# Performance work log

Measured on AMD Instinct MI355X. Metric: run time of the kernel, lower is better.

The kernel has to match this reference:

```python
import jax, jax.numpy as jnp
import numpy as np

def setup_inputs() -> dict:
    key = jax.random.key(0)
    k1, k2, k3, k4 = jax.random.split(key, 4)
    B, S, E, H = 4, 4096, 1024, 64
    x = jax.random.normal(k1, (B, S, E), dtype=jnp.float32)
    scale = E ** -0.5  # keep activations well-scaled like trained Linear weights
    Wq = jax.random.normal(k2, (E, H), dtype=jnp.float32) * scale
    Wk = jax.random.normal(k3, (E, H), dtype=jnp.float32) * scale
    Wv = jax.random.normal(k4, (E, H), dtype=jnp.float32) * scale
    return {"x": x, "Wq": Wq, "Wk": Wk, "Wv": Wv}

def reference(x, Wq, Wk, Wv):
    # x: [B, S, E]; W*: [E, H]
    B, S, E = x.shape
    H = Wq.shape[1]
    q = jnp.einsum('bse,eh->bsh', x, Wq)
    k = jnp.einsum('bse,eh->bsh', x, Wk)
    v = jnp.einsum('bse,eh->bsh', x, Wv)
    att = jnp.einsum('bqh,bkh->bqk', q, k) * (H ** -0.5)  # [B, S, S]
    causal = jnp.tril(jnp.ones((S, S), dtype=bool))
    att = jnp.where(causal, att, -jnp.inf)
    att = jax.nn.softmax(att, axis=-1)
    # dropout p=0.0 (eval-mode): identity
    return jnp.einsum('bqk,bkh->bqh', att, v)
```

## Files before the change

kernel.cpp:

```cpp
#include <hip/hip_runtime.h>


using short8 = __attribute__((ext_vector_type(8))) short;
using f32x4  = __attribute__((ext_vector_type(4))) float;

#define MFMA16(A, B, C) __builtin_amdgcn_mfma_f32_16x16x32_bf16((A), (B), (C), 0, 0, 0)

typedef const __attribute__((address_space(1))) void* gas_ptr;
typedef __attribute__((address_space(3))) void*       las_ptr;

__device__ __forceinline__ void gload16(const void* g, void* l) {
    __builtin_amdgcn_global_load_lds((gas_ptr)g, (las_ptr)l, 16, 0, 0);
}

__device__ __forceinline__ unsigned short f2bf(float f) {
    unsigned u = __builtin_bit_cast(unsigned, f);
    u += 0x7fffu + ((u >> 16) & 1u);
    return (unsigned short)(u >> 16);
}
__device__ __forceinline__ float bf2f(unsigned short u) {
    unsigned v = ((unsigned)u) << 16;
    return __builtin_bit_cast(float, v);
}

__device__ __forceinline__ float exp2_fast(float x) {
#if __has_builtin(__builtin_amdgcn_exp2f)
    return __builtin_amdgcn_exp2f(x);
#else
    float r;
    asm("v_exp_f32 %0, %1" : "=v"(r) : "v"(x));
    return r;
#endif
}

__global__ __launch_bounds__(256) void transpose_w(
    const float* __restrict__ Wq,
    const float* __restrict__ Wk,
    const float* __restrict__ Wv,
    unsigned short* __restrict__ Ws)
{
    int o = blockIdx.x * 256 + threadIdx.x;
    if (o < 196608) {
        int j    = o & 7;
        int l    = (o >> 3) & 63;
        int g    = (o >> 9) & 7;
        int rem  = o >> 12;
        int mt   = rem % 3;
        int sk   = rem / 3;
        int c    = g >> 2, nt = g & 3;
        int quad = l >> 4, n  = l & 15;
        int e    = sk * 64 + c * 32 + quad * 8 + j;
        int h    = nt * 16 + n;
        const float* W = (mt == 0) ? Wq : (mt == 1) ? Wk : Wv;
        Ws[o] = f2bf(W[e * 64 + h]);
    }
}

__global__ __launch_bounds__(128, 2) void proj_all(
    const float* __restrict__ x,
    const unsigned short* __restrict__ Ws,
    unsigned short* __restrict__ Qo,
    unsigned short* __restrict__ Ko,
    unsigned short* __restrict__ Vto)
{
    const int m0   = blockIdx.x * 32;
    const int tid  = threadIdx.x;
    const int lane = tid & 63;
    const int wv   = tid >> 6;
    const int quad = lane >> 4;
    const int n    = lane & 15;

    __shared__ __align__(16) float xs[2][8][64][4];
    __shared__ __align__(16) short wf[2][24][64][8];

    const f32x4 zero4 = {0.f, 0.f, 0.f, 0.f};
    f32x4 acc[3][4];
    #pragma unroll
    for (int mt = 0; mt < 3; ++mt)
        #pragma unroll
        for (int nt = 0; nt < 4; ++nt) acc[mt][nt] = zero4;

    auto stage = [&](int k0, int p) {
        #pragma unroll
        for (int it = 0; it < 4; ++it) {
            int i     = wv + 2 * it;
            int Rl    = 4 * i + (lane >> 4);
            int chunk = (lane & 15) ^ ((Rl & 3) << 2);
            gload16(x + (size_t)(m0 + Rl) * 1024 + k0 + chunk * 4, &xs[p][i][0][0]);
        }
        int sk = k0 >> 6;
        #pragma unroll
        for (int it = 0; it < 12; ++it) {
            int f = wv + 2 * it;
            gload16(Ws + (((size_t)sk * 24 + f) << 9) + lane * 8, &wf[p][f][0][0]);
        }
    };

    int p = 0;
    stage(0, 0);
    __syncthreads();

    for (int k0 = 0; k0 < 1024; k0 += 64) {
        if (k0 < 960) stage(k0 + 64, p ^ 1);

        int sub = n & 3, s = sub << 2;
        const float* xp = &xs[p][wv * 4 + (n >> 2)][0][0] + sub * 64;
        f32x4 u0 = *(const f32x4*)(xp + (((2 * quad)     ^ s) << 2));
        f32x4 u1 = *(const f32x4*)(xp + (((2 * quad + 1) ^ s) << 2));
        f32x4 u2 = *(const f32x4*)(xp + (((8 + 2 * quad) ^ s) << 2));
        f32x4 u3 = *(const f32x4*)(xp + (((9 + 2 * quad) ^ s) << 2));
        short8 a0, a1;
        #pragma unroll
        for (int j = 0; j < 4; ++j) {
            a0[j]     = (short)f2bf(u0[j]);
            a0[4 + j] = (short)f2bf(u1[j]);
            a1[j]     = (short)f2bf(u2[j]);
            a1[4 + j] = (short)f2bf(u3[j]);
        }

        #pragma unroll
        for (int mt = 0; mt < 3; ++mt)
            #pragma unroll
            for (int nt = 0; nt < 4; ++nt) {
                acc[mt][nt] = MFMA16(a0, *(const short8*)(&wf[p][mt * 8 + nt][lane][0]),     acc[mt][nt]);
                acc[mt][nt] = MFMA16(a1, *(const short8*)(&wf[p][mt * 8 + 4 + nt][lane][0]), acc[mt][nt]);
            }

        __syncthreads();
        p ^= 1;
    }

    #pragma unroll
    for (int nt = 0; nt < 4; ++nt) {
        #pragma unroll
        for (int r = 0; r < 4; ++r) {
            int m = m0 + wv * 16 + quad * 4 + r;
            int h = nt * 16 + n;
            Qo[(size_t)m * 64 + h] = f2bf(acc[0][nt][r]);
            Ko[(size_t)m * 64 + h] = f2bf(acc[1][nt][r]);
            int b = m >> 12, s2 = m & 4095;
            Vto[((size_t)(b * 80 + h)) * 4096 + s2] = f2bf(acc[2][nt][r]);
        }
    }
}

template <int SPLIT>
__device__ __forceinline__ void attn_body(
    const unsigned short* __restrict__ Q,
    const unsigned short* __restrict__ K,
    const unsigned short* __restrict__ Vt,
    float* __restrict__ dst,
    int b, int r0, int kt0, int kt1)
{
    const int tid  = threadIdx.x;
    const int lane = tid & 63;
    const int wv   = tid >> 6;
    const int quad = lane >> 4;
    const int n    = lane & 15;
    const int ktmask = r0 >> 6;

    __shared__ __align__(16) short kf[2][8][64][8];
    __shared__ __align__(16) short vf[2][8][64][8];
    __shared__ __align__(16) unsigned short pbuf[4][32][72];

    short8 qa[2][2];
    #pragma unroll
    for (int rg = 0; rg < 2; ++rg) {
        const unsigned short* qp =
            Q + (size_t)(b * 4096 + r0 + wv * 32 + rg * 16 + n) * 64 + quad * 8;
        #pragma unroll
        for (int j = 0; j < 8; ++j) {
            qa[rg][0][j] = (short)f2bf(bf2f(qp[j])      * 0.18033688f);
            qa[rg][1][j] = (short)f2bf(bf2f(qp[32 + j]) * 0.18033688f);
        }
    }

    const f32x4 zero4 = {0.f, 0.f, 0.f, 0.f};
    f32x4 oacc[2][4];
    float lacc[2][4];
    #pragma unroll
    for (int rg = 0; rg < 2; ++rg)
        #pragma unroll
        for (int nt = 0; nt < 4; ++nt) { oacc[rg][nt] = zero4; lacc[rg][nt] = 0.f; }

    const unsigned short* kbase = K  + ((size_t)b * 4096 + n) * 64 + quad * 8;
    const unsigned short* vbase = Vt + ((size_t)b * 80 + n) * 4096 + quad * 8;

    auto stage = [&](int kt, int p) {
        #pragma unroll
        for (int it = 0; it < 4; ++it) {
            int f = wv + 4 * it;
            if (f < 8) {
                int c = f >> 2, nt = f & 3;
                gload16(kbase + (size_t)(kt * 64 + nt * 16) * 64 + c * 32, &kf[p][f][0][0]);
            } else {
                int pnl = f - 8;
                int nt = pnl >> 1, c = pnl & 1;
                gload16(vbase + (size_t)nt * 16 * 4096 + kt * 64 + c * 32, &vf[p][pnl][0][0]);
            }
        }
    };

    int p = 0;
    stage(kt0, 0);
    __syncthreads();

    for (int kt = kt0; kt <= kt1; ++kt) {
        if (kt < kt1) stage(kt + 1, p ^ 1);

        f32x4 sacc[2][4];
        #pragma unroll
        for (int rg = 0; rg < 2; ++rg)
            #pragma unroll
            for (int nt = 0; nt < 4; ++nt) sacc[rg][nt] = zero4;

        #pragma unroll
        for (int nt = 0; nt < 4; ++nt) {
            short8 ka = *(const short8*)(&kf[p][nt][lane][0]);
            short8 kb = *(const short8*)(&kf[p][4 + nt][lane][0]);
            #pragma unroll
            for (int rg = 0; rg < 2; ++rg) {
                sacc[rg][nt] = MFMA16(qa[rg][0], ka, sacc[rg][nt]);
                sacc[rg][nt] = MFMA16(qa[rg][1], kb, sacc[rg][nt]);
            }
        }

        if (kt >= ktmask) {
            #pragma unroll
            for (int rg = 0; rg < 2; ++rg) {
                int qg = r0 + wv * 32 + rg * 16 + quad * 4;
                #pragma unroll
                for (int nt = 0; nt < 4; ++nt)
                    #pragma unroll
                    for (int r = 0; r < 4; ++r) {
                        int key = kt * 64 + nt * 16 + n;
                        if (key > qg + r) sacc[rg][nt][r] = -1e30f;
                    }
            }
        }

        #pragma unroll
        for (int rg = 0; rg < 2; ++rg)
            #pragma unroll
            for (int r = 0; r < 4; ++r) {
                float rs = 0.f;
                #pragma unroll
                for (int nt = 0; nt < 4; ++nt) {
                    unsigned short pv = f2bf(exp2_fast(sacc[rg][nt][r]));
                    pbuf[wv][rg * 16 + quad * 4 + r][nt * 16 + n] = pv;
                    rs += bf2f(pv);
                }
                lacc[rg][r] += rs;
            }

        short8 pa[2][2];
        #pragma unroll
        for (int rg = 0; rg < 2; ++rg) {
            pa[rg][0] = *(const short8*)(&pbuf[wv][rg * 16 + n][quad * 8]);
            pa[rg][1] = *(const short8*)(&pbuf[wv][rg * 16 + n][32 + quad * 8]);
        }
        #pragma unroll
        for (int nt = 0; nt < 4; ++nt) {
            short8 va = *(const short8*)(&vf[p][2 * nt][lane][0]);
            short8 vb = *(const short8*)(&vf[p][2 * nt + 1][lane][0]);
            #pragma unroll
            for (int rg = 0; rg < 2; ++rg) {
                oacc[rg][nt] = MFMA16(pa[rg][0], va, oacc[rg][nt]);
                oacc[rg][nt] = MFMA16(pa[rg][1], vb, oacc[rg][nt]);
            }
        }

        __syncthreads();
        p ^= 1;
    }

    #pragma unroll
    for (int rg = 0; rg < 2; ++rg)
        #pragma unroll
        for (int r = 0; r < 4; ++r) {
            float v = lacc[rg][r];
            v += __shfl_xor(v, 1);
            v += __shfl_xor(v, 2);
            v += __shfl_xor(v, 4);
            v += __shfl_xor(v, 8);
            lacc[rg][r] = v;
        }

    if (SPLIT) {
        #pragma unroll
        for (int rg = 0; rg < 2; ++rg)
            #pragma unroll
            for (int r = 0; r < 4; ++r) {
                int row = wv * 32 + rg * 16 + quad * 4 + r;
                #pragma unroll
                for (int nt = 0; nt < 4; ++nt)
                    dst[row * 64 + nt * 16 + n] = oacc[rg][nt][r];
                if (n == 0) dst[8192 + row] = lacc[rg][r];
            }
    } else {
        #pragma unroll
        for (int rg = 0; rg < 2; ++rg)
            #pragma unroll
            for (int r = 0; r < 4; ++r) {
                float inv = 1.f / lacc[rg][r];
                int q = r0 + wv * 32 + rg * 16 + quad * 4 + r;
                #pragma unroll
                for (int nt = 0; nt < 4; ++nt)
                    dst[(size_t)(b * 4096 + q) * 64 + nt * 16 + n] = oacc[rg][nt][r] * inv;
            }
    }
}

__global__ __launch_bounds__(256, 3) void attn_part(
    const unsigned short* __restrict__ Q,
    const unsigned short* __restrict__ K,
    const unsigned short* __restrict__ Vt,
    float* __restrict__ Part)
{
    int id = blockIdx.x;
    int b  = id & 3;
    int t  = 143 - (id >> 2);
    int g  = 0;
    while (2 * (g + 1) * (g + 2) <= t) ++g;
    int u  = t - 2 * g * (g + 1);
    int qt = 4 * g + u / (g + 1);
    int c  = u - (u / (g + 1)) * (g + 1);

    int r0  = qt * 128;
    int kt0 = c * 8;
    int kt1 = min(kt0 + 7, 2 * qt + 1);

    float* dst = Part + (size_t)(b * 144 + t) * 8320;
    attn_body<1>(Q, K, Vt, dst, b, r0, kt0, kt1);
}

__global__ __launch_bounds__(256, 3) void attn_mono(
    const unsigned short* __restrict__ Q,
    const unsigned short* __restrict__ K,
    const unsigned short* __restrict__ Vt,
    float* __restrict__ out)
{
    int id = blockIdx.x;
    int qt = 31 - (id >> 2);
    int b  = id & 3;
    attn_body<0>(Q, K, Vt, out, b, qt * 128, 0, 2 * qt + 1);
}

__global__ __launch_bounds__(256) void combine(
    const float* __restrict__ Part, float* __restrict__ out)
{
    int id    = blockIdx.x;
    int slice = id & 3;
    int bq    = id >> 2;
    int b     = bq & 3;
    int qt    = bq >> 2;
    int g     = qt >> 2;
    int nc    = g + 1;
    int t0    = 2 * g * (g + 1) + (qt & 3) * (g + 1);
    const float* P0 = Part + (size_t)(b * 144 + t0) * 8320;

    int tid = threadIdx.x;

    __shared__ float invden[32];
    if (tid < 32) {
        float d[8] = {0, 0, 0, 0, 0, 0, 0, 0};
        #pragma unroll 8
        for (int c = 0; c < 8; ++c)
            if (c < nc) d[c] = P0[c * 8320 + 8192 + slice * 32 + tid];
        invden[tid] = 1.f / (((d[0] + d[1]) + (d[2] + d[3])) +
                             ((d[4] + d[5]) + (d[6] + d[7])));
    }

    float acc[8] = {0, 0, 0, 0, 0, 0, 0, 0};
    const float* Pe = P0 + slice * 2048 + tid;
    for (int c = 0; c < nc; ++c) {
        const float* Pc = Pe + (size_t)c * 8320;
        #pragma unroll
        for (int j = 0; j < 8; ++j)
            acc[j] += Pc[j * 256];
    }

    __syncthreads();
    #pragma unroll
    for (int j = 0; j < 8; ++j) {
        int e   = slice * 2048 + j * 256 + tid;
        int row = (e >> 6) & 31;
        out[((size_t)b * 4096 + qt * 128 + slice * 32) * 64 + (size_t)(j * 256 + tid)]
            = acc[j] * invden[row];
    }
}

extern "C" void kernel_launch(void* const* d_in, const int* in_sizes, int n_in,
                              void* d_out, int out_size, void* d_ws, size_t ws_size,
                              hipStream_t stream) {
    const float* x  = (const float*)d_in[0];
    const float* Wq = (const float*)d_in[1];
    const float* Wk = (const float*)d_in[2];
    const float* Wv = (const float*)d_in[3];
    float* outp = (float*)d_out;
    unsigned short* ws = (unsigned short*)d_ws;

    unsigned short* Qw  = ws;
    unsigned short* Kw  = ws + 1048576;
    unsigned short* Vtw = ws + 2097152;
    unsigned short* Wsp = ws + 3407872;

    size_t part_off = ((size_t)3604480 * 2 + 255) & ~(size_t)255;
    size_t need     = part_off + (size_t)4 * 144 * 8320 * 4;
    float* Part = (float*)((char*)d_ws + part_off);

    transpose_w<<<dim3(768), dim3(256), 0, stream>>>(Wq, Wk, Wv, Wsp);
    proj_all<<<dim3(512), dim3(128), 0, stream>>>(x, Wsp, Qw, Kw, Vtw);

    if (ws_size >= need) {
        attn_part<<<dim3(576), dim3(256), 0, stream>>>(Qw, Kw, Vtw, Part);
        combine<<<dim3(512), dim3(256), 0, stream>>>(Part, outp);
    } else {
        attn_mono<<<dim3(128), dim3(256), 0, stream>>>(Qw, Kw, Vtw, outp);
    }
}
```

Before: 149.4 us.

## Restructure projection to 4 waves with register-prefetched x and add MFMA priority hints

The projection kernel now runs 256 threads per block, with each wave computing half of the head columns for 16 rows. The x tile is no longer staged through LDS; it is loaded directly into registers one k-step ahead, and only W goes through LDS double buffering. The attention loop also wraps its MFMA sections in s_setprio so matrix work gets scheduling priority. The trade is that each x row is now loaded twice (once per column-half wave) and register pressure rises in exchange for less LDS traffic and more waves.

```diff
diff --git a/kernel.cpp b/kernel.cpp
--- a/kernel.cpp
+++ b/kernel.cpp
@@ -56,7 +56,7 @@
     }
 }
 
-__global__ __launch_bounds__(128, 2) void proj_all(
+__global__ __launch_bounds__(256, 2) void proj_all(
     const float* __restrict__ x,
     const unsigned short* __restrict__ Ws,
     unsigned short* __restrict__ Qo,
@@ -67,79 +67,85 @@
     const int tid  = threadIdx.x;
     const int lane = tid & 63;
     const int wv   = tid >> 6;
+    const int rt   = wv & 1;
+    const int ch   = wv >> 1;
     const int quad = lane >> 4;
     const int n    = lane & 15;
 
-    __shared__ __align__(16) float xs[2][8][64][4];
     __shared__ __align__(16) short wf[2][24][64][8];
 
     const f32x4 zero4 = {0.f, 0.f, 0.f, 0.f};
-    f32x4 acc[3][4];
+    f32x4 acc[3][2];
     #pragma unroll
     for (int mt = 0; mt < 3; ++mt)
         #pragma unroll
-        for (int nt = 0; nt < 4; ++nt) acc[mt][nt] = zero4;
-
-    auto stage = [&](int k0, int p) {
-        #pragma unroll
-        for (int it = 0; it < 4; ++it) {
-            int i     = wv + 2 * it;
-            int Rl    = 4 * i + (lane >> 4);
-            int chunk = (lane & 15) ^ ((Rl & 3) << 2);
-            gload16(x + (size_t)(m0 + Rl) * 1024 + k0 + chunk * 4, &xs[p][i][0][0]);
-        }
+        for (int ntl = 0; ntl < 2; ++ntl) acc[mt][ntl] = zero4;
+
+    const float* xrow = x + (size_t)(m0 + rt * 16 + n) * 1024 + 8 * quad;
+
+    auto stageW = [&](int k0, int p) {
         int sk = k0 >> 6;
         #pragma unroll
-        for (int it = 0; it < 12; ++it) {
-            int f = wv + 2 * it;
+        for (int it = 0; it < 6; ++it) {
+            int f = wv + 4 * it;
             gload16(Ws + (((size_t)sk * 24 + f) << 9) + lane * 8, &wf[p][f][0][0]);
         }
     };
 
-    int p = 0;
-    stage(0, 0);
+    f32x4 ua[4], ub[4];
+    #pragma unroll
+    for (int j = 0; j < 4; ++j) {
+        const float* s = xrow + ((j & 1) ? 4 : 0) + ((j >> 1) ? 32 : 0);
+        ua[j] = *(const f32x4*)s;
+    }
+    stageW(0, 0);
     __syncthreads();
 
-    for (int k0 = 0; k0 < 1024; k0 += 64) {
-        if (k0 < 960) stage(k0 + 64, p ^ 1);
-
-        int sub = n & 3, s = sub << 2;
-        const float* xp = &xs[p][wv * 4 + (n >> 2)][0][0] + sub * 64;
-        f32x4 u0 = *(const f32x4*)(xp + (((2 * quad)     ^ s) << 2));
-        f32x4 u1 = *(const f32x4*)(xp + (((2 * quad + 1) ^ s) << 2));
-        f32x4 u2 = *(const f32x4*)(xp + (((8 + 2 * quad) ^ s) << 2));
-        f32x4 u3 = *(const f32x4*)(xp + (((9 + 2 * quad) ^ s) << 2));
+    auto body = [&](int k0, f32x4 (&uc)[4], f32x4 (&un)[4], int pp) {
+        int nk = (k0 < 960) ? k0 + 64 : 0;
+        #pragma unroll
+        for (int j = 0; j < 4; ++j) {
+            const float* s = xrow + nk + ((j & 1) ? 4 : 0) + ((j >> 1) ? 32 : 0);
+            un[j] = *(const f32x4*)s;
+        }
+        if (k0 < 960) stageW(k0 + 64, pp ^ 1);
+
         short8 a0, a1;
         #pragma unroll
         for (int j = 0; j < 4; ++j) {
-            a0[j]     = (short)f2bf(u0[j]);
-            a0[4 + j] = (short)f2bf(u1[j]);
-            a1[j]     = (short)f2bf(u2[j]);
-            a1[4 + j] = (short)f2bf(u3[j]);
+            a0[j]     = (short)f2bf(uc[0][j]);
+            a0[4 + j] = (short)f2bf(uc[1][j]);
+            a1[j]     = (short)f2bf(uc[2][j]);
+            a1[4 + j] = (short)f2bf(uc[3][j]);
         }
 
         #pragma unroll
         for (int mt = 0; mt < 3; ++mt)
             #pragma unroll
-            for (int nt = 0; nt < 4; ++nt) {
-                acc[mt][nt] = MFMA16(a0, *(const short8*)(&wf[p][mt * 8 + nt][lane][0]),     acc[mt][nt]);
-                acc[mt][nt] = MFMA16(a1, *(const short8*)(&wf[p][mt * 8 + 4 + nt][lane][0]), acc[mt][nt]);
+            for (int ntl = 0; ntl < 2; ++ntl) {
+                int nt = 2 * ch + ntl;
+                acc[mt][ntl] = MFMA16(a0, *(const short8*)(&wf[pp][mt * 8 + nt][lane][0]),     acc[mt][ntl]);
+                acc[mt][ntl] = MFMA16(a1, *(const short8*)(&wf[pp][mt * 8 + 4 + nt][lane][0]), acc[mt][ntl]);
             }
 
         __syncthreads();
-        p ^= 1;
-    }
-
-    #pragma unroll
-    for (int nt = 0; nt < 4; ++nt) {
+    };
+
+    for (int k0 = 0; k0 < 1024; k0 += 128) {
+        body(k0,      ua, ub, 0);
+        body(k0 + 64, ub, ua, 1);
+    }
+
+    #pragma unroll
+    for (int ntl = 0; ntl < 2; ++ntl) {
+        int h = (2 * ch + ntl) * 16 + n;
         #pragma unroll
         for (int r = 0; r < 4; ++r) {
-            int m = m0 + wv * 16 + quad * 4 + r;
-            int h = nt * 16 + n;
-            Qo[(size_t)m * 64 + h] = f2bf(acc[0][nt][r]);
-            Ko[(size_t)m * 64 + h] = f2bf(acc[1][nt][r]);
+            int m = m0 + rt * 16 + quad * 4 + r;
+            Qo[(size_t)m * 64 + h] = f2bf(acc[0][ntl][r]);
+            Ko[(size_t)m * 64 + h] = f2bf(acc[1][ntl][r]);
             int b = m >> 12, s2 = m & 4095;
-            Vto[((size_t)(b * 80 + h)) * 4096 + s2] = f2bf(acc[2][nt][r]);
+            Vto[((size_t)(b * 80 + h)) * 4096 + s2] = f2bf(acc[2][ntl][r]);
         }
     }
 }
@@ -214,6 +220,7 @@
             #pragma unroll
             for (int nt = 0; nt < 4; ++nt) sacc[rg][nt] = zero4;
 
+        __builtin_amdgcn_s_setprio(1);
         #pragma unroll
         for (int nt = 0; nt < 4; ++nt) {
             short8 ka = *(const short8*)(&kf[p][nt][lane][0]);
@@ -224,6 +231,7 @@
                 sacc[rg][nt] = MFMA16(qa[rg][1], kb, sacc[rg][nt]);
             }
         }
+        __builtin_amdgcn_s_setprio(0);
 
         if (kt >= ktmask) {
             #pragma unroll
@@ -259,6 +267,7 @@
             pa[rg][0] = *(const short8*)(&pbuf[wv][rg * 16 + n][quad * 8]);
             pa[rg][1] = *(const short8*)(&pbuf[wv][rg * 16 + n][32 + quad * 8]);
         }
+        __builtin_amdgcn_s_setprio(1);
         #pragma unroll
         for (int nt = 0; nt < 4; ++nt) {
             short8 va = *(const short8*)(&vf[p][2 * nt][lane][0]);
@@ -269,6 +278,7 @@
                 oacc[rg][nt] = MFMA16(pa[rg][1], vb, oacc[rg][nt]);
             }
         }
+        __builtin_amdgcn_s_setprio(0);
 
         __syncthreads();
         p ^= 1;
@@ -410,7 +420,7 @@
     float* Part = (float*)((char*)d_ws + part_off);
 
     transpose_w<<<dim3(768), dim3(256), 0, stream>>>(Wq, Wk, Wv, Wsp);
-    proj_all<<<dim3(512), dim3(128), 0, stream>>>(x, Wsp, Qw, Kw, Vtw);
+    proj_all<<<dim3(512), dim3(256), 0, stream>>>(x, Wsp, Qw, Kw, Vtw);
 
     if (ws_size >= need) {
         attn_part<<<dim3(576), dim3(256), 0, stream>>>(Qw, Kw, Vtw, Part);
```

Result: slower. 154.6 us (+3.5%).
